# Kernel optimization log

Hardware: AMD Instinct MI355X
Metric: run time of the kernel (lower is better)

## Reference

```python
import jax, jax.numpy as jnp
import numpy as np

V_FEATS = 1024; N1 = 800; N2 = 800; K = 10
CONV = [256, 128]; DENSE = [256, 64]


def setup_inputs() -> dict:
    key = jax.random.key(0)
    ks = jax.random.split(key, 20)
    inp = {
        "Z1": jax.random.normal(ks[0], (N1, V_FEATS), jnp.float32),
        "nb1": jax.random.randint(ks[2], (N1, K), -1, N1),
        "Z2": jax.random.normal(ks[1], (N2, V_FEATS), jnp.float32),
        "nb2": jax.random.randint(ks[3], (N2, K), -1, N2),
    }
    j = 4
    dims = [V_FEATS] + CONV
    for i, (di, do) in enumerate(zip(dims[:-1], dims[1:])):
        s = 1.0 / np.sqrt(di)
        inp[f"Wr{i}"] = jax.random.normal(ks[j], (di, do), jnp.float32) * s; j += 1
        inp[f"Wnr{i}"] = jax.random.normal(ks[j], (di, do), jnp.float32) * s; j += 1
    fdims = [2 * CONV[-1]] + DENSE + [1]
    for i, (di, do) in enumerate(zip(fdims[:-1], fdims[1:])):
        s = 1.0 / np.sqrt(di)
        inp[f"fW{i}"] = jax.random.normal(ks[j], (di, do), jnp.float32) * s; j += 1
        inp[f"fb{i}"] = jnp.zeros((do,), jnp.float32)
    return inp


def gnn_layer(Z, nb, Wr, Wnr):
    # residue (self) signal and neighbor base signal
    res = Z @ Wr                                  # [N, F]
    base = Z @ Wnr                                # [N, F]
    mask = nb > -1                                # [N, K]
    feats = base[nb] * mask[..., None]            # gather (neg idx wrap, masked out)
    norm = jnp.maximum(mask.sum(1), 1).astype(Z.dtype)  # [N], avoid div-by-0
    return jax.nn.relu(res + feats.sum(1) / norm[:, None])


def _forward(Z1, nb1, Z2, nb2, Wr0, Wnr0, Wr1, Wnr1, fW0, fb0, fW1, fb1, fW2, fb2):
    # two stacked GNN layers per protein (shared weights across the two proteins)
    x1 = gnn_layer(gnn_layer(Z1, nb1, Wr0, Wnr0), nb1, Wr1, Wnr1)  # [N1, F]
    x2 = gnn_layer(gnn_layer(Z2, nb2, Wr0, Wnr0), nb2, Wr1, Wnr1)  # [N2, F]
    n1, F = x1.shape
    n2 = x2.shape[0]
    # all-pairs concat: itertools.product(rows(x1), rows(x2)) -> [N1*N2, 2F]
    pairs = jnp.concatenate(
        [jnp.broadcast_to(x1[:, None, :], (n1, n2, F)),
         jnp.broadcast_to(x2[None, :, :], (n1, n2, F))], axis=-1
    ).reshape(n1 * n2, 2 * F)
    h = jax.nn.relu(pairs @ fW0 + fb0)
    h = jax.nn.relu(h @ fW1 + fb1)
    return jnp.squeeze(h @ fW2 + fb2)             # [N1*N2]


def reference(Z1, nb1, Z2, nb2, Wr0, Wnr0, Wr1, Wnr1, fW0, fb0, fW1, fb1, fW2, fb2):
    return _forward(Z1, nb1, Z2, nb2, Wr0, Wnr0, Wr1, Wnr1,
                    fW0, fb0, fW1, fb1, fW2, fb2)
```

## Files before the change

kernel.cpp:

```cpp
#include <hip/hip_runtime.h>
#include <hip/hip_bf16.h>
#include <cstdint>
#include <cstddef>


typedef __bf16 bf16_t;
typedef __bf16 bf16x4 __attribute__((ext_vector_type(4)));
typedef __bf16 bf16x8 __attribute__((ext_vector_type(8)));
typedef float f32x4 __attribute__((ext_vector_type(4)));
typedef _Float16 f16_t;
typedef _Float16 f16x8 __attribute__((ext_vector_type(8)));

static __device__ __forceinline__ f32x4 mfma_bf16(bf16x8 a, bf16x8 b, f32x4 c) {
  return __builtin_amdgcn_mfma_f32_16x16x32_bf16(a, b, c, 0, 0, 0);
}
static __device__ __forceinline__ f32x4 mfma_f16(f16x8 a, f16x8 b, f32x4 c) {
  return __builtin_amdgcn_mfma_f32_16x16x32_f16(a, b, c, 0, 0, 0);
}

#define N1R 800
#define NR  1600
#define VF  1024
#define F0  256
#define F1  128

static __device__ __forceinline__ void split8(float4 va, float4 vb,
                                              bf16x8& h8, bf16x8& l8) {
  float v[8] = {va.x, va.y, va.z, va.w, vb.x, vb.y, vb.z, vb.w};
  #pragma unroll
  for (int e = 0; e < 8; ++e) {
    bf16_t h = (bf16_t)v[e];
    h8[e] = h;
    l8[e] = (bf16_t)(v[e] - (float)h);
  }
}

__global__ void conv_agg(const float* __restrict__ Z1, const float* __restrict__ Z2,
                         const int* __restrict__ nb1, const int* __restrict__ nb2,
                         const float* __restrict__ Wr0, const float* __restrict__ Wnr0,
                         const float* __restrict__ Wr1, const float* __restrict__ Wnr1,
                         const float* __restrict__ fW0, const float* __restrict__ fW1,
                         const float* __restrict__ fb1, const float* __restrict__ fW2,
                         const float* __restrict__ fb2,
                         bf16_t* __restrict__ W0h, bf16_t* __restrict__ W0l,
                         bf16_t* __restrict__ W1h, bf16_t* __restrict__ W1l,
                         bf16_t* __restrict__ fAh, bf16_t* __restrict__ fAl,
                         bf16_t* __restrict__ fBh, bf16_t* __restrict__ fBl,
                         f16_t* __restrict__ fW1th, float* __restrict__ fbw,
                         bf16_t* __restrict__ Zah, bf16_t* __restrict__ Zal) {
  int wb = blockIdx.x;
  int tid = threadIdx.x;
  if (wb >= 2625) {
    int r = wb - 2625;
    const int* nbp;
    const float* Zp;
    if (r < N1R) { nbp = nb1 + r * 10; Zp = Z1; }
    else         { nbp = nb2 + (r - N1R) * 10; Zp = Z2; }
    int c4 = tid * 4;
    float4 s = make_float4(0.f, 0.f, 0.f, 0.f);
    int cnt = 0;
    #pragma unroll
    for (int k = 0; k < 10; ++k) {
      int idx = nbp[k];
      if (idx > -1) {
        cnt++;
        float4 v = *(const float4*)(Zp + (size_t)idx * VF + c4);
        s.x += v.x; s.y += v.y; s.z += v.z; s.w += v.w;
      }
    }
    float inv = 1.f / (float)(cnt > 0 ? cnt : 1);
    float vv[4] = {s.x * inv, s.y * inv, s.z * inv, s.w * inv};
    bf16x4 h4, l4;
    #pragma unroll
    for (int e = 0; e < 4; ++e) {
      bf16_t h = (bf16_t)vv[e];
      h4[e] = h;
      l4[e] = (bf16_t)(vv[e] - (float)h);
    }
    *(bf16x4*)(Zah + (size_t)r * VF + c4) = h4;
    *(bf16x4*)(Zal + (size_t)r * VF + c4) = l4;
    return;
  }
  if (wb >= 2560 && wb < 2624) {
    int t = (wb - 2560) * 256 + tid;
    int n = t & 63;
    int k = t >> 6;
    fW1th[(n << 8) + k] = (f16_t)fW1[k * 64 + n];
    return;
  }
  if (wb == 2624) {
    if (tid < 128) {
      int jl = tid & 15, s = tid >> 4;
      fbw[jl * 8 + s] = (s < 4) ? fb1[s * 16 + jl] : fW2[(s - 4) * 16 + jl];
    } else if (tid == 128) {
      fbw[128] = fb2[0];
    }
    return;
  }
  const float* src; bf16_t* dh; bf16_t* dl; int ld, lk, ln, b0;
  if      (wb < 1024) { src = Wr0;  ld = 256; lk = 10; ln = 8; dh = W0h;              dl = W0l;              b0 = 0;    }
  else if (wb < 2048) { src = Wnr0; ld = 256; lk = 10; ln = 8; dh = W0h + 256 * 1024; dl = W0l + 256 * 1024; b0 = 1024; }
  else if (wb < 2176) { src = Wr1;  ld = 128; lk = 8;  ln = 7; dh = W1h;              dl = W1l;              b0 = 2048; }
  else if (wb < 2304) { src = Wnr1; ld = 128; lk = 8;  ln = 7; dh = W1h + 128 * 256;  dl = W1l + 128 * 256;  b0 = 2176; }
  else if (wb < 2432) { src = fW0;             ld = 256; lk = 7; ln = 8; dh = fAh;    dl = fAl;              b0 = 2304; }
  else                { src = fW0 + 128 * 256; ld = 256; lk = 7; ln = 8; dh = fBh;    dl = fBl;              b0 = 2432; }
  int t = (wb - b0) * 256 + tid;
  int n = t & ((1 << ln) - 1);
  int k = t >> ln;
  float v = src[k * ld + n];
  bf16_t h = (bf16_t)v;
  dh[(n << lk) + k] = h;
  dl[(n << lk) + k] = (bf16_t)(v - (float)h);
}

__global__ __launch_bounds__(256) void gemm_l1(
    const float* __restrict__ Z1, const float* __restrict__ Z2,
    const bf16_t* __restrict__ Zah, const bf16_t* __restrict__ Zal,
    const bf16_t* __restrict__ W0h, const bf16_t* __restrict__ W0l,
    float* __restrict__ P) {
  int lane = threadIdx.x & 63;
  int w = threadIdx.x >> 6;
  int jl = lane & 15, hi = lane >> 4;

  int row0 = blockIdx.y * 16;
  int col = blockIdx.x * 64 + w * 16 + jl;
  int z = blockIdx.z;
  int r = row0 + jl;

  const size_t WOFF = (size_t)z * 256 * 1024;
  const bf16_t* pBh = W0h + WOFF + (size_t)col * 1024 + hi * 8;
  const bf16_t* pBl = W0l + WOFF + (size_t)col * 1024 + hi * 8;

  f32x4 acc = {};
  if (z == 0) {
    const float* pZ = ((r < N1R) ? Z1 + (size_t)r * VF
                                 : Z2 + (size_t)(r - N1R) * VF) + hi * 8;
    #pragma unroll 4
    for (int kb = 0; kb < 1024; kb += 32) {
      bf16x8 ah, al;
      split8(*(const float4*)(pZ + kb), *(const float4*)(pZ + kb + 4), ah, al);
      bf16x8 bh = *(const bf16x8*)(pBh + kb);
      bf16x8 bl = *(const bf16x8*)(pBl + kb);
      acc = mfma_bf16(ah, bh, acc);
      acc = mfma_bf16(al, bh, acc);
      acc = mfma_bf16(ah, bl, acc);
    }
  } else {
    const bf16_t* pAh = Zah + (size_t)r * VF + hi * 8;
    const bf16_t* pAl = Zal + (size_t)r * VF + hi * 8;
    #pragma unroll 4
    for (int kb = 0; kb < 1024; kb += 32) {
      bf16x8 ah = *(const bf16x8*)(pAh + kb);
      bf16x8 al = *(const bf16x8*)(pAl + kb);
      bf16x8 bh = *(const bf16x8*)(pBh + kb);
      bf16x8 bl = *(const bf16x8*)(pBl + kb);
      acc = mfma_bf16(ah, bh, acc);
      acc = mfma_bf16(al, bh, acc);
      acc = mfma_bf16(ah, bl, acc);
    }
  }
  float* Pz = P + (size_t)z * NR * F0;
  #pragma unroll
  for (int reg = 0; reg < 4; ++reg) {
    int row = row0 + hi * 4 + reg;
    Pz[(size_t)row * F0 + col] = acc[reg];
  }
}

__global__ void agg1_kernel(const float* __restrict__ P,
                            const int* __restrict__ nb1, const int* __restrict__ nb2,
                            bf16_t* __restrict__ H0h, bf16_t* __restrict__ H0l,
                            bf16_t* __restrict__ Gah, bf16_t* __restrict__ Gal) {
  int r = blockIdx.x;
  int c = threadIdx.x;
  const float* P1 = P + (size_t)NR * F0;
  const int* nbp;
  int roff;
  if (r < N1R) { nbp = nb1 + r * 10; roff = 0; }
  else         { nbp = nb2 + (r - N1R) * 10; roff = N1R; }
  size_t so = (size_t)r * F0 + c;
  float v = fmaxf(P[so] + P1[so], 0.f);
  bf16_t h = (bf16_t)v;
  H0h[so] = h;
  H0l[so] = (bf16_t)(v - (float)h);
  float s = 0.f; int cnt = 0;
  #pragma unroll
  for (int k = 0; k < 10; ++k) {
    int idx = nbp[k];
    if (idx > -1) {
      cnt++;
      size_t o = (size_t)(roff + idx) * F0 + c;
      s += fmaxf(P[o] + P1[o], 0.f);
    }
  }
  float g = s / (float)(cnt > 0 ? cnt : 1);
  bf16_t gh = (bf16_t)g;
  Gah[so] = gh;
  Gal[so] = (bf16_t)(g - (float)gh);
}

__global__ __launch_bounds__(256) void gemm_l2(
    const bf16_t* __restrict__ H0h, const bf16_t* __restrict__ H0l,
    const bf16_t* __restrict__ Gah, const bf16_t* __restrict__ Gal,
    const bf16_t* __restrict__ W1h, const bf16_t* __restrict__ W1l,
    bf16_t* __restrict__ H1h, bf16_t* __restrict__ H1l) {
  int lane = threadIdx.x & 63;
  int w = threadIdx.x >> 6;
  int jl = lane & 15, hi = lane >> 4;

  int row0 = blockIdx.y * 16;
  int col = blockIdx.x * 64 + w * 16 + jl;
  int r = row0 + jl;

  const bf16_t* pAh = H0h + (size_t)r * F0 + hi * 8;
  const bf16_t* pAl = H0l + (size_t)r * F0 + hi * 8;
  const bf16_t* pGh = Gah + (size_t)r * F0 + hi * 8;
  const bf16_t* pGl = Gal + (size_t)r * F0 + hi * 8;
  const bf16_t* pBh = W1h + (size_t)col * 256 + hi * 8;
  const bf16_t* pBl = W1l + (size_t)col * 256 + hi * 8;
  const size_t OFF = (size_t)128 * 256;

  f32x4 acc = {};
  #pragma unroll 2
  for (int kb = 0; kb < 256; kb += 32) {
    bf16x8 ah = *(const bf16x8*)(pAh + kb);
    bf16x8 al = *(const bf16x8*)(pAl + kb);
    bf16x8 bh = *(const bf16x8*)(pBh + kb);
    bf16x8 bl = *(const bf16x8*)(pBl + kb);
    acc = mfma_bf16(ah, bh, acc);
    acc = mfma_bf16(al, bh, acc);
    acc = mfma_bf16(ah, bl, acc);
  }
  #pragma unroll 2
  for (int kb = 0; kb < 256; kb += 32) {
    bf16x8 ah = *(const bf16x8*)(pGh + kb);
    bf16x8 al = *(const bf16x8*)(pGl + kb);
    bf16x8 bh = *(const bf16x8*)(pBh + OFF + kb);
    bf16x8 bl = *(const bf16x8*)(pBl + OFF + kb);
    acc = mfma_bf16(ah, bh, acc);
    acc = mfma_bf16(al, bh, acc);
    acc = mfma_bf16(ah, bl, acc);
  }

  #pragma unroll
  for (int reg = 0; reg < 4; ++reg) {
    int row = row0 + hi * 4 + reg;
    float v = fmaxf(acc[reg], 0.f);
    bf16_t h = (bf16_t)v;
    H1h[(size_t)row * F1 + col] = h;
    H1l[(size_t)row * F1 + col] = (bf16_t)(v - (float)h);
  }
}

__global__ __launch_bounds__(256) void gemm_dual(
    const bf16_t* __restrict__ H1h, const bf16_t* __restrict__ H1l,
    const bf16_t* __restrict__ fAh, const bf16_t* __restrict__ fAl,
    const bf16_t* __restrict__ fBh, const bf16_t* __restrict__ fBl,
    const float* __restrict__ fb0, f16_t* __restrict__ ABh) {
  int lane = threadIdx.x & 63;
  int w = threadIdx.x >> 6;
  int jl = lane & 15, hi = lane >> 4;

  int part = blockIdx.y / 50;
  int my = blockIdx.y % 50;
  int row0 = my * 16;
  int col = blockIdx.x * 64 + w * 16 + jl;
  int r = row0 + jl;

  const bf16_t* Ah = H1h + (size_t)part * N1R * F1;
  const bf16_t* Al = H1l + (size_t)part * N1R * F1;
  const bf16_t* Bh = part ? fBh : fAh;
  const bf16_t* Bl = part ? fBl : fAl;

  const bf16_t* pAh = Ah + (size_t)r * F1 + hi * 8;
  const bf16_t* pAl = Al + (size_t)r * F1 + hi * 8;
  const bf16_t* pBh = Bh + (size_t)col * F1 + hi * 8;
  const bf16_t* pBl = Bl + (size_t)col * F1 + hi * 8;

  f32x4 acc = {};
  #pragma unroll
  for (int kb = 0; kb < 128; kb += 32) {
    bf16x8 ah = *(const bf16x8*)(pAh + kb);
    bf16x8 al = *(const bf16x8*)(pAl + kb);
    bf16x8 bh = *(const bf16x8*)(pBh + kb);
    bf16x8 bl = *(const bf16x8*)(pBl + kb);
    acc = mfma_bf16(ah, bh, acc);
    acc = mfma_bf16(al, bh, acc);
    acc = mfma_bf16(ah, bl, acc);
  }

  float bv = part ? 0.f : fb0[col];
  f16_t* C = ABh + (size_t)part * N1R * 256;
  #pragma unroll
  for (int reg = 0; reg < 4; ++reg) {
    int row = row0 + hi * 4 + reg;
    C[(size_t)row * 256 + col] = (f16_t)(acc[reg] + bv);
  }
}

#define IBLK 2
#define ITILE 16
__global__ __launch_bounds__(256) void pair_kernel(
    const f16_t* __restrict__ ABh, const f16_t* __restrict__ W1th,
    const float* __restrict__ fbw, float* __restrict__ out) {
  __shared__ alignas(16) unsigned char sWh[64 * 512];
  __shared__ alignas(16) f16_t sA[ITILE * 256];

  const int tid = threadIdx.x;
  const int lane = tid & 63;
  const int w = tid >> 6;
  const int jl = lane & 15;
  const int hi = lane >> 4;
  const int j0 = blockIdx.x * 64;
  const int i0 = blockIdx.y * ITILE;

  #pragma unroll
  for (int s = 0; s < 8; ++s) {
    int c = tid + 256 * s;
    int n = c >> 5;
    int cb = (c & 31) << 4;
    int sw = cb ^ ((n & 7) << 4);
    *(uint4*)(sWh + n * 512 + sw) = *(const uint4*)((const unsigned char*)W1th + n * 512 + cb);
  }
  #pragma unroll
  for (int s = 0; s < 2; ++s) {
    int c = tid + 256 * s;
    int rr = c >> 5;
    int cc = c & 31;
    *(uint4*)((unsigned char*)sA + rr * 512 + cc * 16) =
        *(const uint4*)(ABh + (size_t)(i0 + rr) * 256 + cc * 8);
  }

  int j = j0 + w * 16 + jl;
  f16x8 breg[8];
  {
    const f16_t* Bp = ABh + (size_t)(N1R + j) * 256;
    bool ok = (j < N1R);
    f16x8 z{};
    #pragma unroll
    for (int t = 0; t < 8; ++t)
      breg[t] = ok ? *(const f16x8*)(Bp + t * 32 + hi * 8) : z;
  }

  float4 fb1r = *(const float4*)(fbw + jl * 8);
  float4 fw2r = *(const float4*)(fbw + jl * 8 + 4);
  float bias2 = fbw[128];

  __syncthreads();

  #pragma unroll 1
  for (int ig = 0; ig < ITILE / IBLK; ++ig) {
    f32x4 acc[IBLK][4] = {};
    #pragma unroll
    for (int t = 0; t < 8; ++t) {
      f16x8 bv = breg[t];
      f16x8 af[IBLK];
      const f16x8 Zv{};
      #pragma unroll
      for (int ib = 0; ib < IBLK; ++ib) {
        f16x8 av = *(const f16x8*)(sA + (ig * IBLK + ib) * 256 + t * 32 + hi * 8);
        af[ib] = __builtin_elementwise_max(av + bv, Zv);
      }
      int kbyte = t * 64 + hi * 16;
      #pragma unroll
      for (int nf = 0; nf < 4; ++nf) {
        int n = nf * 16 + jl;
        f16x8 wh = *(const f16x8*)(sWh + n * 512 + (kbyte ^ ((n & 7) << 4)));
        #pragma unroll
        for (int ib = 0; ib < IBLK; ++ib)
          acc[ib][nf] = mfma_f16(af[ib], wh, acc[ib][nf]);
      }
    }
    float fb1a[4] = {fb1r.x, fb1r.y, fb1r.z, fb1r.w};
    float fw2a[4] = {fw2r.x, fw2r.y, fw2r.z, fw2r.w};
    #pragma unroll
    for (int ib = 0; ib < IBLK; ++ib) {
      float part[4];
      #pragma unroll
      for (int r = 0; r < 4; ++r) {
        float ssum = 0.f;
        #pragma unroll
        for (int nf = 0; nf < 4; ++nf) {
          float h = acc[ib][nf][r] + fb1a[nf];
          h = fmaxf(h, 0.f);
          ssum += h * fw2a[nf];
        }
        part[r] = ssum;
      }
      #pragma unroll
      for (int off = 1; off < 16; off <<= 1) {
        #pragma unroll
        for (int r = 0; r < 4; ++r) part[r] += __shfl_xor(part[r], off, 64);
      }
      if (jl == 0) {
        int jo = j0 + w * 16 + hi * 4;
        if (jo < N1R) {
          float4 o = make_float4(part[0] + bias2, part[1] + bias2,
                                 part[2] + bias2, part[3] + bias2);
          *(float4*)(out + (size_t)(i0 + ig * IBLK + ib) * 800 + jo) = o;
        }
      }
    }
  }
}

extern "C" void kernel_launch(void* const* d_in, const int* in_sizes, int n_in,
                              void* d_out, int out_size, void* d_ws, size_t ws_size,
                              hipStream_t stream) {
  const float* Z1   = (const float*)d_in[0];
  const int*   nb1  = (const int*)d_in[1];
  const float* Z2   = (const float*)d_in[2];
  const int*   nb2  = (const int*)d_in[3];
  const float* Wr0  = (const float*)d_in[4];
  const float* Wnr0 = (const float*)d_in[5];
  const float* Wr1  = (const float*)d_in[6];
  const float* Wnr1 = (const float*)d_in[7];
  const float* fW0  = (const float*)d_in[8];
  const float* fb0  = (const float*)d_in[9];
  const float* fW1  = (const float*)d_in[10];
  const float* fb1  = (const float*)d_in[11];
  const float* fW2  = (const float*)d_in[12];
  const float* fb2  = (const float*)d_in[13];
  float* out = (float*)d_out;

  char* p = (char*)d_ws;
  auto alloc = [&](size_t bytes) {
    char* q = p;
    p += (bytes + 255) & ~(size_t)255;
    return q;
  };
  bf16_t* W0h   = (bf16_t*)alloc((size_t)512 * 1024 * 2);
  bf16_t* W0l   = (bf16_t*)alloc((size_t)512 * 1024 * 2);
  bf16_t* W1h   = (bf16_t*)alloc((size_t)256 * 256 * 2);
  bf16_t* W1l   = (bf16_t*)alloc((size_t)256 * 256 * 2);
  bf16_t* fAh   = (bf16_t*)alloc((size_t)256 * 128 * 2);
  bf16_t* fAl   = (bf16_t*)alloc((size_t)256 * 128 * 2);
  bf16_t* fBh   = (bf16_t*)alloc((size_t)256 * 128 * 2);
  bf16_t* fBl   = (bf16_t*)alloc((size_t)256 * 128 * 2);
  f16_t*  fW1th = (f16_t*)alloc((size_t)64 * 256 * 2);
  float*  fbw   = (float*)alloc(129 * 4);
  bf16_t* Zah   = (bf16_t*)alloc((size_t)NR * VF * 2);
  bf16_t* Zal   = (bf16_t*)alloc((size_t)NR * VF * 2);
  float*  P01   = (float*)alloc((size_t)2 * NR * F0 * 4);
  bf16_t* H0h   = (bf16_t*)alloc((size_t)NR * F0 * 2);
  bf16_t* H0l   = (bf16_t*)alloc((size_t)NR * F0 * 2);
  bf16_t* Gah   = (bf16_t*)alloc((size_t)NR * F0 * 2);
  bf16_t* Gal   = (bf16_t*)alloc((size_t)NR * F0 * 2);
  bf16_t* H1h   = (bf16_t*)alloc((size_t)NR * F1 * 2);
  bf16_t* H1l   = (bf16_t*)alloc((size_t)NR * F1 * 2);
  f16_t*  ABh   = (f16_t*)alloc((size_t)NR * 256 * 2);
  (void)in_sizes; (void)n_in; (void)out_size; (void)ws_size;

  conv_agg<<<4225, 256, 0, stream>>>(Z1, Z2, nb1, nb2, Wr0, Wnr0, Wr1, Wnr1,
                                     fW0, fW1, fb1, fW2, fb2,
                                     W0h, W0l, W1h, W1l, fAh, fAl, fBh, fBl,
                                     fW1th, fbw, Zah, Zal);
  gemm_l1<<<dim3(4, 100, 2), 256, 0, stream>>>(Z1, Z2, Zah, Zal, W0h, W0l, P01);
  agg1_kernel<<<NR, 256, 0, stream>>>(P01, nb1, nb2, H0h, H0l, Gah, Gal);
  gemm_l2<<<dim3(2, 100), 256, 0, stream>>>(H0h, H0l, Gah, Gal, W1h, W1l, H1h, H1l);
  gemm_dual<<<dim3(4, 100), 256, 0, stream>>>(H1h, H1l, fAh, fAl, fBh, fBl, fb0, ABh);
  pair_kernel<<<dim3(13, 50), 256, 0, stream>>>(ABh, fW1th, fbw, out);
}
```

Baseline: 130.1 us.

## Split-K the layer GEMMs and batch loads with dual accumulators

The first-layer GEMM is split along K into two halves, doubling its grid. The partial sums are written separately and added inside the aggregation kernel. The second-layer GEMM is split by its two K segments (self and neighbor) into separate partial buffers, and the following dense GEMM now sums them, applies ReLU and splits to bf16 on the fly. Loads are batched four steps ahead, and even and odd steps feed separate accumulators to expose memory-level parallelism and shorten MFMA dependency chains. This adds fp32 partial-buffer traffic and extra reads in the consuming kernels in exchange for more blocks on the GPU.

```diff
diff --git a/kernel.cpp b/kernel.cpp
--- a/kernel.cpp
+++ b/kernel.cpp
@@ -125,45 +125,64 @@
   int row0 = blockIdx.y * 16;
   int col = blockIdx.x * 64 + w * 16 + jl;
   int z = blockIdx.z;
+  int half = z >> 1;
+  int kStart = (z & 1) * 512;
   int r = row0 + jl;
 
-  const size_t WOFF = (size_t)z * 256 * 1024;
-  const bf16_t* pBh = W0h + WOFF + (size_t)col * 1024 + hi * 8;
-  const bf16_t* pBl = W0l + WOFF + (size_t)col * 1024 + hi * 8;
-
-  f32x4 acc = {};
-  if (z == 0) {
+  const size_t WOFF = (size_t)half * 256 * 1024;
+  const bf16_t* pBh = W0h + WOFF + (size_t)col * 1024 + hi * 8 + kStart;
+  const bf16_t* pBl = W0l + WOFF + (size_t)col * 1024 + hi * 8 + kStart;
+
+  f32x4 accE = {}, accO = {};
+  if (half == 0) {
     const float* pZ = ((r < N1R) ? Z1 + (size_t)r * VF
-                                 : Z2 + (size_t)(r - N1R) * VF) + hi * 8;
-    #pragma unroll 4
-    for (int kb = 0; kb < 1024; kb += 32) {
-      bf16x8 ah, al;
-      split8(*(const float4*)(pZ + kb), *(const float4*)(pZ + kb + 4), ah, al);
-      bf16x8 bh = *(const bf16x8*)(pBh + kb);
-      bf16x8 bl = *(const bf16x8*)(pBl + kb);
-      acc = mfma_bf16(ah, bh, acc);
-      acc = mfma_bf16(al, bh, acc);
-      acc = mfma_bf16(ah, bl, acc);
+                                 : Z2 + (size_t)(r - N1R) * VF) + hi * 8 + kStart;
+    for (int kb = 0; kb < 512; kb += 128) {
+      float4 za[4][2];
+      bf16x8 bh[4], bl[4];
+      #pragma unroll
+      for (int u = 0; u < 4; ++u) {
+        za[u][0] = *(const float4*)(pZ + kb + u * 32);
+        za[u][1] = *(const float4*)(pZ + kb + u * 32 + 4);
+        bh[u] = *(const bf16x8*)(pBh + kb + u * 32);
+        bl[u] = *(const bf16x8*)(pBl + kb + u * 32);
+      }
+      #pragma unroll
+      for (int u = 0; u < 4; ++u) {
+        bf16x8 ah, al;
+        split8(za[u][0], za[u][1], ah, al);
+        f32x4& acc = (u & 1) ? accO : accE;
+        acc = mfma_bf16(ah, bh[u], acc);
+        acc = mfma_bf16(al, bh[u], acc);
+        acc = mfma_bf16(ah, bl[u], acc);
+      }
     }
   } else {
-    const bf16_t* pAh = Zah + (size_t)r * VF + hi * 8;
-    const bf16_t* pAl = Zal + (size_t)r * VF + hi * 8;
-    #pragma unroll 4
-    for (int kb = 0; kb < 1024; kb += 32) {
-      bf16x8 ah = *(const bf16x8*)(pAh + kb);
-      bf16x8 al = *(const bf16x8*)(pAl + kb);
-      bf16x8 bh = *(const bf16x8*)(pBh + kb);
-      bf16x8 bl = *(const bf16x8*)(pBl + kb);
-      acc = mfma_bf16(ah, bh, acc);
-      acc = mfma_bf16(al, bh, acc);
-      acc = mfma_bf16(ah, bl, acc);
+    const bf16_t* pAh = Zah + (size_t)r * VF + hi * 8 + kStart;
+    const bf16_t* pAl = Zal + (size_t)r * VF + hi * 8 + kStart;
+    for (int kb = 0; kb < 512; kb += 128) {
+      bf16x8 ah[4], al[4], bh[4], bl[4];
+      #pragma unroll
+      for (int u = 0; u < 4; ++u) {
+        ah[u] = *(const bf16x8*)(pAh + kb + u * 32);
+        al[u] = *(const bf16x8*)(pAl + kb + u * 32);
+        bh[u] = *(const bf16x8*)(pBh + kb + u * 32);
+        bl[u] = *(const bf16x8*)(pBl + kb + u * 32);
+      }
+      #pragma unroll
+      for (int u = 0; u < 4; ++u) {
+        f32x4& acc = (u & 1) ? accO : accE;
+        acc = mfma_bf16(ah[u], bh[u], acc);
+        acc = mfma_bf16(al[u], bh[u], acc);
+        acc = mfma_bf16(ah[u], bl[u], acc);
+      }
     }
   }
   float* Pz = P + (size_t)z * NR * F0;
   #pragma unroll
   for (int reg = 0; reg < 4; ++reg) {
     int row = row0 + hi * 4 + reg;
-    Pz[(size_t)row * F0 + col] = acc[reg];
+    Pz[(size_t)row * F0 + col] = accE[reg] + accO[reg];
   }
 }
 
@@ -173,13 +192,13 @@
                             bf16_t* __restrict__ Gah, bf16_t* __restrict__ Gal) {
   int r = blockIdx.x;
   int c = threadIdx.x;
-  const float* P1 = P + (size_t)NR * F0;
+  const size_t PS = (size_t)NR * F0;
   const int* nbp;
   int roff;
   if (r < N1R) { nbp = nb1 + r * 10; roff = 0; }
   else         { nbp = nb2 + (r - N1R) * 10; roff = N1R; }
   size_t so = (size_t)r * F0 + c;
-  float v = fmaxf(P[so] + P1[so], 0.f);
+  float v = fmaxf(P[so] + P[so + PS] + P[so + 2 * PS] + P[so + 3 * PS], 0.f);
   bf16_t h = (bf16_t)v;
   H0h[so] = h;
   H0l[so] = (bf16_t)(v - (float)h);
@@ -190,7 +209,7 @@
     if (idx > -1) {
       cnt++;
       size_t o = (size_t)(roff + idx) * F0 + c;
-      s += fmaxf(P[o] + P1[o], 0.f);
+      s += fmaxf(P[o] + P[o + PS] + P[o + 2 * PS] + P[o + 3 * PS], 0.f);
     }
   }
   float g = s / (float)(cnt > 0 ? cnt : 1);
@@ -203,57 +222,50 @@
     const bf16_t* __restrict__ H0h, const bf16_t* __restrict__ H0l,
     const bf16_t* __restrict__ Gah, const bf16_t* __restrict__ Gal,
     const bf16_t* __restrict__ W1h, const bf16_t* __restrict__ W1l,
-    bf16_t* __restrict__ H1h, bf16_t* __restrict__ H1l) {
+    float* __restrict__ P2) {
   int lane = threadIdx.x & 63;
   int w = threadIdx.x >> 6;
   int jl = lane & 15, hi = lane >> 4;
 
   int row0 = blockIdx.y * 16;
   int col = blockIdx.x * 64 + w * 16 + jl;
+  int z = blockIdx.z;
   int r = row0 + jl;
 
-  const bf16_t* pAh = H0h + (size_t)r * F0 + hi * 8;
-  const bf16_t* pAl = H0l + (size_t)r * F0 + hi * 8;
-  const bf16_t* pGh = Gah + (size_t)r * F0 + hi * 8;
-  const bf16_t* pGl = Gal + (size_t)r * F0 + hi * 8;
-  const bf16_t* pBh = W1h + (size_t)col * 256 + hi * 8;
-  const bf16_t* pBl = W1l + (size_t)col * 256 + hi * 8;
-  const size_t OFF = (size_t)128 * 256;
-
-  f32x4 acc = {};
-  #pragma unroll 2
-  for (int kb = 0; kb < 256; kb += 32) {
-    bf16x8 ah = *(const bf16x8*)(pAh + kb);
-    bf16x8 al = *(const bf16x8*)(pAl + kb);
-    bf16x8 bh = *(const bf16x8*)(pBh + kb);
-    bf16x8 bl = *(const bf16x8*)(pBl + kb);
-    acc = mfma_bf16(ah, bh, acc);
-    acc = mfma_bf16(al, bh, acc);
-    acc = mfma_bf16(ah, bl, acc);
-  }
-  #pragma unroll 2
-  for (int kb = 0; kb < 256; kb += 32) {
-    bf16x8 ah = *(const bf16x8*)(pGh + kb);
-    bf16x8 al = *(const bf16x8*)(pGl + kb);
-    bf16x8 bh = *(const bf16x8*)(pBh + OFF + kb);
-    bf16x8 bl = *(const bf16x8*)(pBl + OFF + kb);
-    acc = mfma_bf16(ah, bh, acc);
-    acc = mfma_bf16(al, bh, acc);
-    acc = mfma_bf16(ah, bl, acc);
-  }
-
+  const bf16_t* pAh = (z ? Gah : H0h) + (size_t)r * F0 + hi * 8;
+  const bf16_t* pAl = (z ? Gal : H0l) + (size_t)r * F0 + hi * 8;
+  const size_t WOFF = (size_t)z * 128 * 256;
+  const bf16_t* pBh = W1h + WOFF + (size_t)col * 256 + hi * 8;
+  const bf16_t* pBl = W1l + WOFF + (size_t)col * 256 + hi * 8;
+
+  f32x4 accE = {}, accO = {};
+  for (int kb = 0; kb < 256; kb += 128) {
+    bf16x8 ah[4], al[4], bh[4], bl[4];
+    #pragma unroll
+    for (int u = 0; u < 4; ++u) {
+      ah[u] = *(const bf16x8*)(pAh + kb + u * 32);
+      al[u] = *(const bf16x8*)(pAl + kb + u * 32);
+      bh[u] = *(const bf16x8*)(pBh + kb + u * 32);
+      bl[u] = *(const bf16x8*)(pBl + kb + u * 32);
+    }
+    #pragma unroll
+    for (int u = 0; u < 4; ++u) {
+      f32x4& acc = (u & 1) ? accO : accE;
+      acc = mfma_bf16(ah[u], bh[u], acc);
+      acc = mfma_bf16(al[u], bh[u], acc);
+      acc = mfma_bf16(ah[u], bl[u], acc);
+    }
+  }
+  float* Pz = P2 + (size_t)z * NR * F1;
   #pragma unroll
   for (int reg = 0; reg < 4; ++reg) {
     int row = row0 + hi * 4 + reg;
-    float v = fmaxf(acc[reg], 0.f);
-    bf16_t h = (bf16_t)v;
-    H1h[(size_t)row * F1 + col] = h;
-    H1l[(size_t)row * F1 + col] = (bf16_t)(v - (float)h);
+    Pz[(size_t)row * F1 + col] = accE[reg] + accO[reg];
   }
 }
 
 __global__ __launch_bounds__(256) void gemm_dual(
-    const bf16_t* __restrict__ H1h, const bf16_t* __restrict__ H1l,
+    const float* __restrict__ P2,
     const bf16_t* __restrict__ fAh, const bf16_t* __restrict__ fAl,
     const bf16_t* __restrict__ fBh, const bf16_t* __restrict__ fBl,
     const float* __restrict__ fb0, f16_t* __restrict__ ABh) {
@@ -261,40 +273,51 @@
   int w = threadIdx.x >> 6;
   int jl = lane & 15, hi = lane >> 4;
 
-  int part = blockIdx.y / 50;
-  int my = blockIdx.y % 50;
-  int row0 = my * 16;
+  int row0 = blockIdx.y * 16;
   int col = blockIdx.x * 64 + w * 16 + jl;
   int r = row0 + jl;
-
-  const bf16_t* Ah = H1h + (size_t)part * N1R * F1;
-  const bf16_t* Al = H1l + (size_t)part * N1R * F1;
-  const bf16_t* Bh = part ? fBh : fAh;
-  const bf16_t* Bl = part ? fBl : fAl;
-
-  const bf16_t* pAh = Ah + (size_t)r * F1 + hi * 8;
-  const bf16_t* pAl = Al + (size_t)r * F1 + hi * 8;
-  const bf16_t* pBh = Bh + (size_t)col * F1 + hi * 8;
-  const bf16_t* pBl = Bl + (size_t)col * F1 + hi * 8;
-
-  f32x4 acc = {};
-  #pragma unroll
-  for (int kb = 0; kb < 128; kb += 32) {
-    bf16x8 ah = *(const bf16x8*)(pAh + kb);
-    bf16x8 al = *(const bf16x8*)(pAl + kb);
-    bf16x8 bh = *(const bf16x8*)(pBh + kb);
-    bf16x8 bl = *(const bf16x8*)(pBl + kb);
-    acc = mfma_bf16(ah, bh, acc);
-    acc = mfma_bf16(al, bh, acc);
-    acc = mfma_bf16(ah, bl, acc);
-  }
-
-  float bv = part ? 0.f : fb0[col];
-  f16_t* C = ABh + (size_t)part * N1R * 256;
+  bool isA = (row0 < N1R);
+
+  const float* pP0 = P2 + (size_t)r * F1 + hi * 8;
+  const float* pP1 = pP0 + (size_t)NR * F1;
+  const bf16_t* pBh = (isA ? fAh : fBh) + (size_t)col * F1 + hi * 8;
+  const bf16_t* pBl = (isA ? fAl : fBl) + (size_t)col * F1 + hi * 8;
+
+  float4 p0[4][2], p1[4][2];
+  bf16x8 bh[4], bl[4];
+  #pragma unroll
+  for (int u = 0; u < 4; ++u) {
+    p0[u][0] = *(const float4*)(pP0 + u * 32);
+    p0[u][1] = *(const float4*)(pP0 + u * 32 + 4);
+    p1[u][0] = *(const float4*)(pP1 + u * 32);
+    p1[u][1] = *(const float4*)(pP1 + u * 32 + 4);
+    bh[u] = *(const bf16x8*)(pBh + u * 32);
+    bl[u] = *(const bf16x8*)(pBl + u * 32);
+  }
+  f32x4 accE = {}, accO = {};
+  #pragma unroll
+  for (int u = 0; u < 4; ++u) {
+    float4 s0 = make_float4(fmaxf(p0[u][0].x + p1[u][0].x, 0.f),
+                            fmaxf(p0[u][0].y + p1[u][0].y, 0.f),
+                            fmaxf(p0[u][0].z + p1[u][0].z, 0.f),
+                            fmaxf(p0[u][0].w + p1[u][0].w, 0.f));
+    float4 s1 = make_float4(fmaxf(p0[u][1].x + p1[u][1].x, 0.f),
+                            fmaxf(p0[u][1].y + p1[u][1].y, 0.f),
+                            fmaxf(p0[u][1].z + p1[u][1].z, 0.f),
+                            fmaxf(p0[u][1].w + p1[u][1].w, 0.f));
+    bf16x8 ah, al;
+    split8(s0, s1, ah, al);
+    f32x4& acc = (u & 1) ? accO : accE;
+    acc = mfma_bf16(ah, bh[u], acc);
+    acc = mfma_bf16(al, bh[u], acc);
+    acc = mfma_bf16(ah, bl[u], acc);
+  }
+
+  float bv = isA ? fb0[col] : 0.f;
   #pragma unroll
   for (int reg = 0; reg < 4; ++reg) {
     int row = row0 + hi * 4 + reg;
-    C[(size_t)row * 256 + col] = (f16_t)(acc[reg] + bv);
+    ABh[(size_t)row * 256 + col] = (f16_t)(accE[reg] + accO[reg] + bv);
   }
 }
 
@@ -441,13 +464,12 @@
   float*  fbw   = (float*)alloc(129 * 4);
   bf16_t* Zah   = (bf16_t*)alloc((size_t)NR * VF * 2);
   bf16_t* Zal   = (bf16_t*)alloc((size_t)NR * VF * 2);
-  float*  P01   = (float*)alloc((size_t)2 * NR * F0 * 4);
+  float*  P01   = (float*)alloc((size_t)4 * NR * F0 * 4);
   bf16_t* H0h   = (bf16_t*)alloc((size_t)NR * F0 * 2);
   bf16_t* H0l   = (bf16_t*)alloc((size_t)NR * F0 * 2);
   bf16_t* Gah   = (bf16_t*)alloc((size_t)NR * F0 * 2);
   bf16_t* Gal   = (bf16_t*)alloc((size_t)NR * F0 * 2);
-  bf16_t* H1h   = (bf16_t*)alloc((size_t)NR * F1 * 2);
-  bf16_t* H1l   = (bf16_t*)alloc((size_t)NR * F1 * 2);
+  float*  P2    = (float*)alloc((size_t)2 * NR * F1 * 4);
   f16_t*  ABh   = (f16_t*)alloc((size_t)NR * 256 * 2);
   (void)in_sizes; (void)n_in; (void)out_size; (void)ws_size;
 
@@ -455,9 +477,9 @@
                                      fW0, fW1, fb1, fW2, fb2,
                                      W0h, W0l, W1h, W1l, fAh, fAl, fBh, fBl,
                                      fW1th, fbw, Zah, Zal);
-  gemm_l1<<<dim3(4, 100, 2), 256, 0, stream>>>(Z1, Z2, Zah, Zal, W0h, W0l, P01);
+  gemm_l1<<<dim3(4, 100, 4), 256, 0, stream>>>(Z1, Z2, Zah, Zal, W0h, W0l, P01);
   agg1_kernel<<<NR, 256, 0, stream>>>(P01, nb1, nb2, H0h, H0l, Gah, Gal);
-  gemm_l2<<<dim3(2, 100), 256, 0, stream>>>(H0h, H0l, Gah, Gal, W1h, W1l, H1h, H1l);
-  gemm_dual<<<dim3(4, 100), 256, 0, stream>>>(H1h, H1l, fAh, fAl, fBh, fBl, fb0, ABh);
+  gemm_l2<<<dim3(2, 100, 2), 256, 0, stream>>>(H0h, H0l, Gah, Gal, W1h, W1l, P2);
+  gemm_dual<<<dim3(4, 100), 256, 0, stream>>>(P2, fAh, fAl, fBh, fBl, fb0, ABh);
   pair_kernel<<<dim3(13, 50), 256, 0, stream>>>(ABh, fW1th, fbw, out);
 }
```

Measured after the change: 125.3 us. 3.7% less time.
